# Optimization experiments

Hardware: AMD Instinct MI355X
Metric: run time of the kernel (lower is better)

## Reference

```python
import jax, jax.numpy as jnp
import numpy as np

B, INPUT_DIM, EMB_DIM = 16384, 2048, 768
DOMAIN_NUM, MEMORY_NUM, TAU = 9, 10, 32.0


def setup_inputs() -> dict:
    key = jax.random.key(0)
    k1, k2, k3, k4, k5 = jax.random.split(key, 5)
    feature = jax.random.normal(k1, (B, INPUT_DIM), dtype=jnp.float32)
    category = jax.random.randint(k2, (B,), 0, DOMAIN_NUM, dtype=jnp.int64)
    # Linear(input_dim, emb_dim, bias=False) weights: [emb_dim, input_dim]
    W_topic = jax.random.normal(k3, (EMB_DIM, INPUT_DIM), dtype=jnp.float32) * 0.02
    W_domain = jax.random.normal(k4, (EMB_DIM, INPUT_DIM), dtype=jnp.float32) * 0.02
    # domain_num Embedding(memory_num, emb_dim) tables, stacked: [D, M, E]
    memory_tables = jax.random.normal(k5, (DOMAIN_NUM, MEMORY_NUM, EMB_DIM), dtype=jnp.float32)
    return {"feature": feature, "W_topic": W_topic, "W_domain": W_domain,
            "memory_tables": memory_tables, "category": category}


def reference(feature, W_topic, W_domain, memory_tables, category):
    eps = 1e-12
    # F.normalize(feature, p=2, dim=-1)
    norm = jnp.maximum(jnp.linalg.norm(feature, axis=-1, keepdims=True), eps)
    feat = feature / norm                                   # [B, I]
    # per-sample gather of each sample's category memory table: [B, M, E]
    mem = memory_tables[category]
    # faithful quirk: loop over domain_num indexes the BATCH dim of the stack
    D = memory_tables.shape[0]
    mems_d = mem[:D]                                        # [D, M, E]
    t = feat @ W_topic.T                                    # [B, E]
    topic_att = jax.nn.softmax(jnp.einsum('be,dme->bdm', t, mems_d) * TAU, axis=-1)
    sep = jnp.einsum('bdm,dme->bde', topic_att, mems_d)     # [B, D, E]
    dproj = feat @ W_domain.T                               # [B, E]
    domain_att = jax.nn.softmax(jnp.einsum('bde,be->bd', sep, dproj) * TAU, axis=-1)
    return domain_att[:, None, :]                           # [B, 1, D]
```

## Files before the change

kernel.cpp:

```cpp
#include <hip/hip_runtime.h>
#include <math.h>

#define TAU_F 32.0f

typedef __attribute__((ext_vector_type(8))) _Float16 half8;
typedef __attribute__((ext_vector_type(4))) float f32x4;

union HU { uint4 u; half8 v; };
union H4 { _Float16 h[4]; uint2 u2; };

__global__ __launch_bounds__(256) void gproj2(
    const float* __restrict__ Wt, const float* __restrict__ Wd,
    const float* __restrict__ mem, const int* __restrict__ cat,
    float* __restrict__ P)
{
    __shared__ float Ml[96 * 36];
    __shared__ float Wl[32 * 68];

    const int bid = blockIdx.x;
    const int mat = bid >> 7;
    const int ks  = (bid >> 5) & 3;
    const int ct  = bid & 31;
    const int c0  = ct * 64;
    const int tid = threadIdx.x;
    const float* __restrict__ W = mat ? Wd : Wt;

    const int tr = tid >> 4;
    const int tc = tid & 15;

    float acc[6][4];
    #pragma unroll
    for (int j = 0; j < 6; ++j)
        #pragma unroll
        for (int q = 0; q < 4; ++q) acc[j][q] = 0.f;

    for (int ch = 0; ch < 6; ++ch) {
        __syncthreads();
        #pragma unroll
        for (int p = 0; p < 3; ++p) {
            const int idx = tid + 256 * p;
            const int r   = idx >> 3;
            const int kq  = idx & 7;
            float4 v = make_float4(0.f, 0.f, 0.f, 0.f);
            if (r < 90) {
                const int d = r / 10;
                const int mrow = cat[d] * 10 + (r - d * 10);
                v = *(const float4*)(mem + (size_t)mrow * 768 + ks * 192 + ch * 32 + kq * 4);
            }
            *(float4*)(Ml + r * 36 + kq * 4) = v;
        }
        #pragma unroll
        for (int p = 0; p < 2; ++p) {
            const int idx = tid + 256 * p;
            const int e   = idx >> 4;
            const int c4  = (idx & 15) * 4;
            *(float4*)(Wl + e * 68 + c4) =
                *(const float4*)(W + (size_t)(ks * 192 + ch * 32 + e) * 2048 + c0 + c4);
        }
        __syncthreads();

        #pragma unroll
        for (int e = 0; e < 32; e += 4) {
            float4 m4[6], w4[4];
            #pragma unroll
            for (int j = 0; j < 6; ++j) m4[j] = *(const float4*)(Ml + (tr * 6 + j) * 36 + e);
            #pragma unroll
            for (int q = 0; q < 4; ++q) w4[q] = *(const float4*)(Wl + (e + q) * 68 + tc * 4);
            #pragma unroll
            for (int j = 0; j < 6; ++j) {
                const float mv[4] = {m4[j].x, m4[j].y, m4[j].z, m4[j].w};
                #pragma unroll
                for (int q = 0; q < 4; ++q) {
                    acc[j][0] = fmaf(mv[q], w4[q].x, acc[j][0]);
                    acc[j][1] = fmaf(mv[q], w4[q].y, acc[j][1]);
                    acc[j][2] = fmaf(mv[q], w4[q].z, acc[j][2]);
                    acc[j][3] = fmaf(mv[q], w4[q].w, acc[j][3]);
                }
            }
        }
    }

    #pragma unroll
    for (int j = 0; j < 6; ++j) {
        float4 v = make_float4(acc[j][0], acc[j][1], acc[j][2], acc[j][3]);
        *(float4*)(P + (size_t)ks * 393216 + (size_t)(mat * 96 + tr * 6 + j) * 2048 + c0 + tc * 4) = v;
    }
}

__global__ __launch_bounds__(256) void split_g3(
    const float* __restrict__ P, unsigned short* __restrict__ gB)
{
    const int u  = blockIdx.x * 256 + threadIdx.x;
    const int n  = u >> 8;
    const int k0 = (u & 255) * 8;

    float s[8] = {0.f, 0.f, 0.f, 0.f, 0.f, 0.f, 0.f, 0.f};
    #pragma unroll
    for (int ks = 0; ks < 4; ++ks) {
        const float4 a = *(const float4*)(P + (size_t)ks * 393216 + (size_t)n * 2048 + k0);
        const float4 b = *(const float4*)(P + (size_t)ks * 393216 + (size_t)n * 2048 + k0 + 4);
        s[0] += a.x; s[1] += a.y; s[2] += a.z; s[3] += a.w;
        s[4] += b.x; s[5] += b.y; s[6] += b.z; s[7] += b.w;
    }
    union { _Float16 h[8]; uint4 u4; } hi, lo;
    #pragma unroll
    for (int e = 0; e < 8; ++e) {
        const _Float16 h = (_Float16)s[e];
        hi.h[e] = h;
        lo.h[e] = (_Float16)(s[e] - (float)h);
    }
    const int kc = k0 >> 5;
    const int lq = (k0 >> 3) & 3;
    const int nq = n / 48;
    const int rm = n - nq * 48;
    const int j  = rm >> 4;
    const int lm = rm & 15;
    const size_t fH = (size_t)((kc * 12 + nq * 3 + j) * 2 + 0) * 512 + lq * 128 + lm * 8;
    const size_t fL = (size_t)((kc * 12 + nq * 3 + j) * 2 + 1) * 512 + lq * 128 + lm * 8;
    *(uint4*)(gB + fH) = hi.u4;
    *(uint4*)(gB + fL) = lo.u4;
}

#define SPAD 196

__global__ __launch_bounds__(256, 2) void fused_mfma3(
    const float* __restrict__ feat, const unsigned short* __restrict__ gB,
    float* __restrict__ out)
{
    __shared__ __align__(16) char smem[25088];
    __shared__ float ssqf[32];
    unsigned short* aS = (unsigned short*)smem;
    float* scores = (float*)smem;

    const int tid  = threadIdx.x;
    const int row0 = blockIdx.x * 32;
    const int nq = tid >> 6, l = tid & 63;
    const int lm = l & 15,  lq = l >> 4;

    const int srow = tid >> 3;
    const int skq  = tid & 7;

    f32x4 acc[2][3];
    #pragma unroll
    for (int i = 0; i < 2; ++i)
        #pragma unroll
        for (int j = 0; j < 3; ++j) acc[i][j] = (f32x4)0.f;
    float ssq = 0.f;

    const float* fptr = feat + (size_t)(row0 + srow) * 2048 + skq * 4;

    const unsigned short* bptr = gB + (size_t)(nq * 3) * 2 * 512 + l * 8;

    float4 fA  = *(const float4*)(fptr);
    float4 fd1 = *(const float4*)(fptr + 32);
    float4 fd2 = *(const float4*)(fptr + 64);
    uint4 bh[3], bl[3];
    #pragma unroll
    for (int j = 0; j < 3; ++j) {
        bh[j] = *(const uint4*)(bptr + j * 1024);
        bl[j] = *(const uint4*)(bptr + j * 1024 + 512);
    }
    {
        const float xs[4] = {fA.x, fA.y, fA.z, fA.w};
        H4 h, lo;
        #pragma unroll
        for (int e = 0; e < 4; ++e) {
            const float x = xs[e];
            ssq = fmaf(x, x, ssq);
            const _Float16 hh = (_Float16)x;
            h.h[e]  = hh;
            lo.h[e] = (_Float16)(x - (float)hh);
        }
        *(uint2*)(aS + (size_t)(0 * 32 + srow) * 40 + skq * 4) = h.u2;
        *(uint2*)(aS + (size_t)(1 * 32 + srow) * 40 + skq * 4) = lo.u2;
    }
    __syncthreads();

    for (int kc = 0; kc < 64; ++kc) {
        const int kf = (kc + 3 < 64) ? kc + 3 : 63;
        float4 fd3 = *(const float4*)(fptr + kf * 32);
        const int kb = (kc + 1 < 64) ? kc + 1 : 63;
        uint4 bhn[3], bln[3];
        #pragma unroll
        for (int j = 0; j < 3; ++j) {
            bhn[j] = *(const uint4*)(bptr + (size_t)kb * 12288 + j * 1024);
            bln[j] = *(const uint4*)(bptr + (size_t)kb * 12288 + j * 1024 + 512);
        }

        if (kc < 63) {
            const int nb = (kc + 1) & 1;
            const float xs[4] = {fd1.x, fd1.y, fd1.z, fd1.w};
            H4 h, lo;
            #pragma unroll
            for (int e = 0; e < 4; ++e) {
                const float x = xs[e];
                ssq = fmaf(x, x, ssq);
                const _Float16 hh = (_Float16)x;
                h.h[e]  = hh;
                lo.h[e] = (_Float16)(x - (float)hh);
            }
            *(uint2*)(aS + (size_t)((nb * 2 + 0) * 32 + srow) * 40 + skq * 4) = h.u2;
            *(uint2*)(aS + (size_t)((nb * 2 + 1) * 32 + srow) * 40 + skq * 4) = lo.u2;
        }

        const int cb = kc & 1;
        half8 fh[2], fl[2];
        #pragma unroll
        for (int i = 0; i < 2; ++i) {
            HU t0, t1;
            t0.u = *(const uint4*)(aS + (size_t)((cb * 2 + 0) * 32 + i * 16 + lm) * 40 + lq * 8);
            t1.u = *(const uint4*)(aS + (size_t)((cb * 2 + 1) * 32 + i * 16 + lm) * 40 + lq * 8);
            fh[i] = t0.v; fl[i] = t1.v;
        }

        #pragma unroll
        for (int j = 0; j < 3; ++j) {
            HU h8, l8; h8.u = bh[j]; l8.u = bl[j];
            #pragma unroll
            for (int i = 0; i < 2; ++i) {
                acc[i][j] = __builtin_amdgcn_mfma_f32_16x16x32_f16(fh[i], h8.v, acc[i][j], 0, 0, 0);
                acc[i][j] = __builtin_amdgcn_mfma_f32_16x16x32_f16(fh[i], l8.v, acc[i][j], 0, 0, 0);
                acc[i][j] = __builtin_amdgcn_mfma_f32_16x16x32_f16(fl[i], h8.v, acc[i][j], 0, 0, 0);
            }
        }
        __syncthreads();

        fd1 = fd2; fd2 = fd3;
        #pragma unroll
        for (int j = 0; j < 3; ++j) { bh[j] = bhn[j]; bl[j] = bln[j]; }
    }

    ssq += __shfl_xor(ssq, 1, 64);
    ssq += __shfl_xor(ssq, 2, 64);
    ssq += __shfl_xor(ssq, 4, 64);
    if ((tid & 7) == 0) ssqf[tid >> 3] = ssq;

    #pragma unroll
    for (int i = 0; i < 2; ++i)
        #pragma unroll
        for (int j = 0; j < 3; ++j)
            #pragma unroll
            for (int r = 0; r < 4; ++r)
                scores[(size_t)(i * 16 + lq * 4 + r) * SPAD + nq * 48 + j * 16 + lm] = acc[i][j][r];
    __syncthreads();

    if (tid < 32) {
        const int r = tid;
        const float inv = TAU_F / fmaxf(sqrtf(ssqf[r]), 1e-12f);
        const float* sc = scores + (size_t)r * SPAD;
        float lg[9];
        float dmax = -1e30f;
        #pragma unroll
        for (int d = 0; d < 9; ++d) {
            const float* v = sc + d * 10;
            const float* u = sc + 96 + d * 10;
            float mx = v[0];
            #pragma unroll
            for (int m = 1; m < 10; ++m) mx = fmaxf(mx, v[m]);
            float s = 0.f, dot = 0.f;
            #pragma unroll
            for (int m = 0; m < 10; ++m) {
                const float p = __expf((v[m] - mx) * inv);
                s += p;
                dot = fmaf(p, u[m], dot);
            }
            const float lgt = (dot / s) * inv;
            lg[d] = lgt;
            dmax = fmaxf(dmax, lgt);
        }
        float s2 = 0.f;
        #pragma unroll
        for (int d = 0; d < 9; ++d) { const float p = __expf(lg[d] - dmax); lg[d] = p; s2 += p; }
        const float r2 = 1.0f / s2;
        #pragma unroll
        for (int d = 0; d < 9; ++d)
            out[(size_t)(row0 + r) * 9 + d] = lg[d] * r2;
    }
}

extern "C" void kernel_launch(void* const* d_in, const int* in_sizes, int n_in,
                              void* d_out, int out_size, void* d_ws, size_t ws_size,
                              hipStream_t stream) {
    const float* feature = (const float*)d_in[0];
    const float* Wt      = (const float*)d_in[1];
    const float* Wd      = (const float*)d_in[2];
    const float* mem     = (const float*)d_in[3];
    const int*   cat     = (const int*)d_in[4];

    float* P = (float*)d_ws;
    unsigned short* gB = (unsigned short*)((char*)d_ws + (size_t)4 * 192 * 2048 * 4);
    float* out = (float*)d_out;

    gproj2<<<256, 256, 0, stream>>>(Wt, Wd, mem, cat, P);
    split_g3<<<192, 256, 0, stream>>>(P, gB);
    fused_mfma3<<<512, 256, 0, stream>>>(feature, gB, out);
}
```

Baseline: 268.2 us.

## Split-K GEMM with 128-row tiles and separate softmax epilogue kernel

```diff
diff --git a/kernel.cpp b/kernel.cpp
--- a/kernel.cpp
+++ b/kernel.cpp
@@ -4,10 +4,10 @@
 #define TAU_F 32.0f
 
 typedef __attribute__((ext_vector_type(8))) _Float16 half8;
+typedef __attribute__((ext_vector_type(2))) __fp16 half2v;
 typedef __attribute__((ext_vector_type(4))) float f32x4;
 
 union HU { uint4 u; half8 v; };
-union H4 { _Float16 h[4]; uint2 u2; };
 
 __global__ __launch_bounds__(256) void gproj2(
     const float* __restrict__ Wt, const float* __restrict__ Wd,
@@ -121,150 +121,208 @@
     *(uint4*)(gB + fL) = lo.u4;
 }
 
-#define SPAD 196
-
-__global__ __launch_bounds__(256, 2) void fused_mfma3(
+__global__ __launch_bounds__(256, 2) void fused_mfma4(
     const float* __restrict__ feat, const unsigned short* __restrict__ gB,
+    float* __restrict__ P2, float* __restrict__ ssqp)
+{
+    __shared__ __align__(16) unsigned short aS[20480];
+
+    const int tid = threadIdx.x;
+    const int rt  = blockIdx.x >> 2;
+    const int ks  = blockIdx.x & 3;
+    const int row0 = rt * 128;
+
+    const int w  = tid >> 6, l = tid & 63;
+    const int lm = l & 15,  lq = l >> 4;
+    const int r8 = tid >> 3, kq = tid & 7;
+
+    f32x4 acc[8][3];
+    #pragma unroll
+    for (int i = 0; i < 8; ++i)
+        #pragma unroll
+        for (int j = 0; j < 3; ++j) acc[i][j] = (f32x4)0.f;
+    float ssq4[4] = {0.f, 0.f, 0.f, 0.f};
+
+    const float* fbase = feat + (size_t)(row0 + r8) * 2048 + ks * 512 + kq * 4;
+    const unsigned short* bbase = gB + (size_t)ks * 196608 + (w * 3) * 1024 + l * 8;
+
+    float4 fa[4], fan[4];
+    #pragma unroll
+    for (int p = 0; p < 4; ++p) fa[p] = *(const float4*)(fbase + p * 65536);
+    uint4 bh0[3], bl0[3], bh1[3], bl1[3];
+    #pragma unroll
+    for (int j = 0; j < 3; ++j) {
+        bh0[j] = *(const uint4*)(bbase + j * 1024);
+        bl0[j] = *(const uint4*)(bbase + j * 1024 + 512);
+        bh1[j] = *(const uint4*)(bbase + 12288 + j * 1024);
+        bl1[j] = *(const uint4*)(bbase + 12288 + j * 1024 + 512);
+    }
+    #pragma unroll
+    for (int p = 0; p < 4; ++p) {
+        const float4 v = fa[p];
+        ssq4[p] = fmaf(v.x, v.x, ssq4[p]); ssq4[p] = fmaf(v.y, v.y, ssq4[p]);
+        ssq4[p] = fmaf(v.z, v.z, ssq4[p]); ssq4[p] = fmaf(v.w, v.w, ssq4[p]);
+        half2v h01 = __builtin_amdgcn_cvt_pkrtz(v.x, v.y);
+        half2v h23 = __builtin_amdgcn_cvt_pkrtz(v.z, v.w);
+        half2v l01 = __builtin_amdgcn_cvt_pkrtz(v.x - (float)h01[0], v.y - (float)h01[1]);
+        half2v l23 = __builtin_amdgcn_cvt_pkrtz(v.z - (float)h23[0], v.w - (float)h23[1]);
+        union { half2v h2[2]; uint2 u2; } uh, ul;
+        uh.h2[0] = h01; uh.h2[1] = h23;
+        ul.h2[0] = l01; ul.h2[1] = l23;
+        const int row = p * 32 + r8;
+        *(uint2*)(aS + 0 * 5120 + row * 40 + kq * 4) = uh.u2;
+        *(uint2*)(aS + 1 * 5120 + row * 40 + kq * 4) = ul.u2;
+    }
+    #pragma unroll
+    for (int p = 0; p < 4; ++p) fan[p] = *(const float4*)(fbase + 32 + p * 65536);
+    __syncthreads();
+
+    #pragma unroll 2
+    for (int kc = 0; kc < 16; ++kc) {
+        const int kn = (kc + 2 < 16) ? kc + 2 : 15;
+        float4 fa2[4];
+        #pragma unroll
+        for (int p = 0; p < 4; ++p) fa2[p] = *(const float4*)(fbase + kn * 32 + p * 65536);
+        uint4 bh2[3], bl2[3];
+        #pragma unroll
+        for (int j = 0; j < 3; ++j) {
+            bh2[j] = *(const uint4*)(bbase + (size_t)kn * 12288 + j * 1024);
+            bl2[j] = *(const uint4*)(bbase + (size_t)kn * 12288 + j * 1024 + 512);
+        }
+
+        if (kc < 15) {
+            const int nb = (kc + 1) & 1;
+            #pragma unroll
+            for (int p = 0; p < 4; ++p) {
+                const float4 v = fan[p];
+                ssq4[p] = fmaf(v.x, v.x, ssq4[p]); ssq4[p] = fmaf(v.y, v.y, ssq4[p]);
+                ssq4[p] = fmaf(v.z, v.z, ssq4[p]); ssq4[p] = fmaf(v.w, v.w, ssq4[p]);
+                half2v h01 = __builtin_amdgcn_cvt_pkrtz(v.x, v.y);
+                half2v h23 = __builtin_amdgcn_cvt_pkrtz(v.z, v.w);
+                half2v l01 = __builtin_amdgcn_cvt_pkrtz(v.x - (float)h01[0], v.y - (float)h01[1]);
+                half2v l23 = __builtin_amdgcn_cvt_pkrtz(v.z - (float)h23[0], v.w - (float)h23[1]);
+                union { half2v h2[2]; uint2 u2; } uh, ul;
+                uh.h2[0] = h01; uh.h2[1] = h23;
+                ul.h2[0] = l01; ul.h2[1] = l23;
+                const int row = p * 32 + r8;
+                *(uint2*)(aS + (nb * 2 + 0) * 5120 + row * 40 + kq * 4) = uh.u2;
+                *(uint2*)(aS + (nb * 2 + 1) * 5120 + row * 40 + kq * 4) = ul.u2;
+            }
+        }
+
+        const int cb = kc & 1;
+        const unsigned short* aH = aS + (cb * 2 + 0) * 5120;
+        const unsigned short* aL = aS + (cb * 2 + 1) * 5120;
+        #pragma unroll
+        for (int ih = 0; ih < 2; ++ih) {
+            half8 fh[4], fl[4];
+            #pragma unroll
+            for (int i2 = 0; i2 < 4; ++i2) {
+                const int row = (ih * 4 + i2) * 16 + lm;
+                HU th, tl;
+                th.u = *(const uint4*)(aH + row * 40 + lq * 8);
+                tl.u = *(const uint4*)(aL + row * 40 + lq * 8);
+                fh[i2] = th.v; fl[i2] = tl.v;
+            }
+            #pragma unroll
+            for (int j = 0; j < 3; ++j) {
+                HU h8, l8; h8.u = bh0[j]; l8.u = bl0[j];
+                #pragma unroll
+                for (int i2 = 0; i2 < 4; ++i2) {
+                    const int i = ih * 4 + i2;
+                    acc[i][j] = __builtin_amdgcn_mfma_f32_16x16x32_f16(fh[i2], h8.v, acc[i][j], 0, 0, 0);
+                    acc[i][j] = __builtin_amdgcn_mfma_f32_16x16x32_f16(fh[i2], l8.v, acc[i][j], 0, 0, 0);
+                    acc[i][j] = __builtin_amdgcn_mfma_f32_16x16x32_f16(fl[i2], h8.v, acc[i][j], 0, 0, 0);
+                }
+            }
+        }
+        __syncthreads();
+
+        #pragma unroll
+        for (int p = 0; p < 4; ++p) fan[p] = fa2[p];
+        #pragma unroll
+        for (int j = 0; j < 3; ++j) {
+            bh0[j] = bh1[j]; bl0[j] = bl1[j];
+            bh1[j] = bh2[j]; bl1[j] = bl2[j];
+        }
+    }
+
+    #pragma unroll
+    for (int p = 0; p < 4; ++p) {
+        float s = ssq4[p];
+        s += __shfl_xor(s, 1, 64);
+        s += __shfl_xor(s, 2, 64);
+        s += __shfl_xor(s, 4, 64);
+        if ((tid & 7) == 0) ssqp[(size_t)ks * 16384 + row0 + p * 32 + r8] = s;
+    }
+
+    #pragma unroll
+    for (int i = 0; i < 8; ++i)
+        #pragma unroll
+        for (int j = 0; j < 3; ++j)
+            #pragma unroll
+            for (int r = 0; r < 4; ++r)
+                P2[((size_t)ks * 16384 + row0 + i * 16 + lq * 4 + r) * 192 + w * 48 + j * 16 + lm]
+                    = acc[i][j][r];
+}
+
+#define EP_SPAD 196
+__global__ __launch_bounds__(256) void ep_kernel(
+    const float* __restrict__ P2, const float* __restrict__ ssqp,
     float* __restrict__ out)
 {
-    __shared__ __align__(16) char smem[25088];
-    __shared__ float ssqf[32];
-    unsigned short* aS = (unsigned short*)smem;
-    float* scores = (float*)smem;
-
+    __shared__ float sc[64 * EP_SPAD];
     const int tid  = threadIdx.x;
-    const int row0 = blockIdx.x * 32;
-    const int nq = tid >> 6, l = tid & 63;
-    const int lm = l & 15,  lq = l >> 4;
-
-    const int srow = tid >> 3;
-    const int skq  = tid & 7;
-
-    f32x4 acc[2][3];
-    #pragma unroll
-    for (int i = 0; i < 2; ++i)
-        #pragma unroll
-        for (int j = 0; j < 3; ++j) acc[i][j] = (f32x4)0.f;
-    float ssq = 0.f;
-
-    const float* fptr = feat + (size_t)(row0 + srow) * 2048 + skq * 4;
-
-    const unsigned short* bptr = gB + (size_t)(nq * 3) * 2 * 512 + l * 8;
-
-    float4 fA  = *(const float4*)(fptr);
-    float4 fd1 = *(const float4*)(fptr + 32);
-    float4 fd2 = *(const float4*)(fptr + 64);
-    uint4 bh[3], bl[3];
-    #pragma unroll
-    for (int j = 0; j < 3; ++j) {
-        bh[j] = *(const uint4*)(bptr + j * 1024);
-        bl[j] = *(const uint4*)(bptr + j * 1024 + 512);
-    }
-    {
-        const float xs[4] = {fA.x, fA.y, fA.z, fA.w};
-        H4 h, lo;
-        #pragma unroll
-        for (int e = 0; e < 4; ++e) {
-            const float x = xs[e];
-            ssq = fmaf(x, x, ssq);
-            const _Float16 hh = (_Float16)x;
-            h.h[e]  = hh;
-            lo.h[e] = (_Float16)(x - (float)hh);
-        }
-        *(uint2*)(aS + (size_t)(0 * 32 + srow) * 40 + skq * 4) = h.u2;
-        *(uint2*)(aS + (size_t)(1 * 32 + srow) * 40 + skq * 4) = lo.u2;
+    const int row0 = blockIdx.x * 64;
+
+    float4 s[12];
+    #pragma unroll
+    for (int p = 0; p < 12; ++p) s[p] = make_float4(0.f, 0.f, 0.f, 0.f);
+    #pragma unroll
+    for (int ks = 0; ks < 4; ++ks)
+        #pragma unroll
+        for (int p = 0; p < 12; ++p) {
+            const int u   = p * 256 + tid;
+            const int row = u / 48;
+            const int c4  = (u - row * 48) * 4;
+            const float4 v = *(const float4*)(P2 + ((size_t)ks * 16384 + row0 + row) * 192 + c4);
+            s[p].x += v.x; s[p].y += v.y; s[p].z += v.z; s[p].w += v.w;
+        }
+    #pragma unroll
+    for (int p = 0; p < 12; ++p) {
+        const int u   = p * 256 + tid;
+        const int row = u / 48;
+        const int c4  = (u - row * 48) * 4;
+        *(float4*)(sc + row * EP_SPAD + c4) = s[p];
+    }
+    float nsq = 0.f;
+    if (tid < 64) {
+        nsq = ssqp[row0 + tid] + ssqp[16384 + row0 + tid]
+            + ssqp[32768 + row0 + tid] + ssqp[49152 + row0 + tid];
     }
     __syncthreads();
 
-    for (int kc = 0; kc < 64; ++kc) {
-        const int kf = (kc + 3 < 64) ? kc + 3 : 63;
-        float4 fd3 = *(const float4*)(fptr + kf * 32);
-        const int kb = (kc + 1 < 64) ? kc + 1 : 63;
-        uint4 bhn[3], bln[3];
-        #pragma unroll
-        for (int j = 0; j < 3; ++j) {
-            bhn[j] = *(const uint4*)(bptr + (size_t)kb * 12288 + j * 1024);
-            bln[j] = *(const uint4*)(bptr + (size_t)kb * 12288 + j * 1024 + 512);
-        }
-
-        if (kc < 63) {
-            const int nb = (kc + 1) & 1;
-            const float xs[4] = {fd1.x, fd1.y, fd1.z, fd1.w};
-            H4 h, lo;
-            #pragma unroll
-            for (int e = 0; e < 4; ++e) {
-                const float x = xs[e];
-                ssq = fmaf(x, x, ssq);
-                const _Float16 hh = (_Float16)x;
-                h.h[e]  = hh;
-                lo.h[e] = (_Float16)(x - (float)hh);
-            }
-            *(uint2*)(aS + (size_t)((nb * 2 + 0) * 32 + srow) * 40 + skq * 4) = h.u2;
-            *(uint2*)(aS + (size_t)((nb * 2 + 1) * 32 + srow) * 40 + skq * 4) = lo.u2;
-        }
-
-        const int cb = kc & 1;
-        half8 fh[2], fl[2];
-        #pragma unroll
-        for (int i = 0; i < 2; ++i) {
-            HU t0, t1;
-            t0.u = *(const uint4*)(aS + (size_t)((cb * 2 + 0) * 32 + i * 16 + lm) * 40 + lq * 8);
-            t1.u = *(const uint4*)(aS + (size_t)((cb * 2 + 1) * 32 + i * 16 + lm) * 40 + lq * 8);
-            fh[i] = t0.v; fl[i] = t1.v;
-        }
-
-        #pragma unroll
-        for (int j = 0; j < 3; ++j) {
-            HU h8, l8; h8.u = bh[j]; l8.u = bl[j];
-            #pragma unroll
-            for (int i = 0; i < 2; ++i) {
-                acc[i][j] = __builtin_amdgcn_mfma_f32_16x16x32_f16(fh[i], h8.v, acc[i][j], 0, 0, 0);
-                acc[i][j] = __builtin_amdgcn_mfma_f32_16x16x32_f16(fh[i], l8.v, acc[i][j], 0, 0, 0);
-                acc[i][j] = __builtin_amdgcn_mfma_f32_16x16x32_f16(fl[i], h8.v, acc[i][j], 0, 0, 0);
-            }
-        }
-        __syncthreads();
-
-        fd1 = fd2; fd2 = fd3;
-        #pragma unroll
-        for (int j = 0; j < 3; ++j) { bh[j] = bhn[j]; bl[j] = bln[j]; }
-    }
-
-    ssq += __shfl_xor(ssq, 1, 64);
-    ssq += __shfl_xor(ssq, 2, 64);
-    ssq += __shfl_xor(ssq, 4, 64);
-    if ((tid & 7) == 0) ssqf[tid >> 3] = ssq;
-
-    #pragma unroll
-    for (int i = 0; i < 2; ++i)
-        #pragma unroll
-        for (int j = 0; j < 3; ++j)
-            #pragma unroll
-            for (int r = 0; r < 4; ++r)
-                scores[(size_t)(i * 16 + lq * 4 + r) * SPAD + nq * 48 + j * 16 + lm] = acc[i][j][r];
-    __syncthreads();
-
-    if (tid < 32) {
+    if (tid < 64) {
         const int r = tid;
-        const float inv = TAU_F / fmaxf(sqrtf(ssqf[r]), 1e-12f);
-        const float* sc = scores + (size_t)r * SPAD;
+        const float inv = TAU_F / fmaxf(sqrtf(nsq), 1e-12f);
+        const float* scr = sc + (size_t)r * EP_SPAD;
         float lg[9];
         float dmax = -1e30f;
         #pragma unroll
         for (int d = 0; d < 9; ++d) {
-            const float* v = sc + d * 10;
-            const float* u = sc + 96 + d * 10;
+            const float* v = scr + d * 10;
+            const float* u = scr + 96 + d * 10;
             float mx = v[0];
             #pragma unroll
             for (int m = 1; m < 10; ++m) mx = fmaxf(mx, v[m]);
-            float s = 0.f, dot = 0.f;
+            float ssum = 0.f, dot = 0.f;
             #pragma unroll
             for (int m = 0; m < 10; ++m) {
                 const float p = __expf((v[m] - mx) * inv);
-                s += p;
+                ssum += p;
                 dot = fmaf(p, u[m], dot);
             }
-            const float lgt = (dot / s) * inv;
+            const float lgt = (dot / ssum) * inv;
             lg[d] = lgt;
             dmax = fmaxf(dmax, lgt);
         }
@@ -287,11 +345,14 @@
     const float* mem     = (const float*)d_in[3];
     const int*   cat     = (const int*)d_in[4];
 
-    float* P = (float*)d_ws;
-    unsigned short* gB = (unsigned short*)((char*)d_ws + (size_t)4 * 192 * 2048 * 4);
+    float* P2 = (float*)d_ws;
+    float* P  = (float*)d_ws;
+    unsigned short* gB = (unsigned short*)((char*)d_ws + 50331648);
+    float* ssqp = (float*)((char*)d_ws + 50331648 + 1572864);
     float* out = (float*)d_out;
 
     gproj2<<<256, 256, 0, stream>>>(Wt, Wd, mem, cat, P);
     split_g3<<<192, 256, 0, stream>>>(P, gB);
-    fused_mfma3<<<512, 256, 0, stream>>>(feature, gB, out);
-}
+    fused_mfma4<<<512, 256, 0, stream>>>(feature, gB, P2, ssqp);
+    ep_kernel<<<256, 256, 0, stream>>>(P2, ssqp, out);
+}
```

New measurement: 251.1 us. -6.4%, faster.
